# Performance work log

Hardware: AMD Instinct MI355X
Metric: run time of the kernel (lower is better)

## Reference

```python
import jax, jax.numpy as jnp
import numpy as np

B, S, I, H, O = 512, 1024, 1, 2048, 128


def _uniform(k, shape, bound):
    return jax.random.uniform(k, shape, jnp.float32, -bound, bound)


def setup_inputs() -> dict:
    key = jax.random.key(0)
    ks = jax.random.split(key, 12)
    gate_bound = 1.0 / np.sqrt(I + H)  # torch nn.Linear default init range
    out_bound = 1.0 / np.sqrt(H)
    return {
        "x": jax.random.normal(ks[0], (B, S, I), jnp.float32),
        "Wg": _uniform(ks[1], (H, I + H), gate_bound),
        "bg": _uniform(ks[2], (H,), gate_bound),
        "Wi": _uniform(ks[3], (H, I + H), gate_bound),
        "bi": _uniform(ks[4], (H,), gate_bound),
        "Wf": _uniform(ks[5], (H, I + H), gate_bound),
        "bf": _uniform(ks[6], (H,), gate_bound),
        "Wo": _uniform(ks[7], (H, I + H), gate_bound),
        "bo": _uniform(ks[8], (H,), gate_bound),
        "Wy": _uniform(ks[9], (O, H), out_bound),
        "by": _uniform(ks[10], (O,), out_bound),
    }


def reference(x, Wg, bg, Wi, bi, Wf, bf, Wo, bo, Wy, by):
    # Batched, scan-over-time LSTM: same math as the original nested Python
    # loops (zero initial h/c, 4 separate gate Linears on concat([x_t, h]),
    # c = g*i + c*f, h = tanh(c)*o, output Linear on the last h).
    b_, h_dim = x.shape[0], Wg.shape[0]
    # Stack the 4 gate weights -> single fused matmul per step. [4H, I+H]
    W = jnp.concatenate([Wg, Wi, Wf, Wo], axis=0)
    b = jnp.concatenate([bg, bi, bf, bo], axis=0)
    h0 = jnp.zeros((b_, h_dim), x.dtype)
    c0 = jnp.zeros((b_, h_dim), x.dtype)

    def step(carry, xt):
        h, c = carry
        xh = jnp.concatenate([xt, h], axis=-1)  # [B, I+H]
        z = xh @ W.T + b                         # [B, 4H]
        g, i, f, o = jnp.split(z, 4, axis=-1)
        g = jnp.tanh(g)
        i = jax.nn.sigmoid(i)
        f = jax.nn.sigmoid(f)
        o = jax.nn.sigmoid(o)
        c = g * i + c * f
        h = jnp.tanh(c) * o
        return (h, c), None

    xs = jnp.swapaxes(x, 0, 1)  # [S, B, I] time-major for scan
    (h_last, _), _ = jax.lax.scan(step, (h0, c0), xs)
    return h_last @ Wy.T + by  # [B, O]
```

## Files before the change

kernel.cpp:

```cpp
#include <hip/hip_runtime.h>

typedef _Float16 f16;
typedef _Float16 f16x8 __attribute__((ext_vector_type(8)));
typedef float f32x4 __attribute__((ext_vector_type(4)));

static constexpr int kS = 1024;

static constexpr size_t OFF_WP = 0;
static constexpr size_t OFF_WX = 33554432;
static constexpr size_t OFF_BB = OFF_WX + 32768;
static constexpr size_t OFF_XT = OFF_BB + 32768;
static constexpr size_t OFF_HA = OFF_XT + 2097152;
static constexpr size_t OFF_HB = OFF_HA + 2097152;
static constexpr size_t OFF_CB = OFF_HB + 2097152;

__device__ __forceinline__ void gload16(const void* g, void* l) {
  __builtin_amdgcn_global_load_lds(
      (const __attribute__((address_space(1))) unsigned int*)g,
      (__attribute__((address_space(3))) unsigned int*)l, 16, 0, 0);
}

__device__ __forceinline__ float sigf(float x) { return 1.f / (1.f + __expf(-x)); }
__device__ __forceinline__ float tanh_fast(float x) {
  float e = __expf(2.f * x);
  return 1.f - 2.f / (e + 1.f);
}

__global__ void pack_weights(const float* __restrict__ Wg, const float* __restrict__ Wi,
                             const float* __restrict__ Wf, const float* __restrict__ Wo,
                             const float* __restrict__ bg, const float* __restrict__ bi,
                             const float* __restrict__ bf, const float* __restrict__ bo,
                             f16* __restrict__ Wp, float* __restrict__ wx, float* __restrict__ bb)
{
  const int R = blockIdx.x;
  const int p = R >> 8, r = R & 255;
  const int u = (p << 6) + (r >> 2), gsel = r & 3;
  const float* Wsrc = (gsel == 0) ? Wg : (gsel == 1) ? Wi : (gsel == 2) ? Wf : Wo;
  const float* bsrc = (gsel == 0) ? bg : (gsel == 1) ? bi : (gsel == 2) ? bf : bo;
  const float* src = Wsrc + (size_t)u * 2049;
  const int k = threadIdx.x * 8;
#pragma unroll
  for (int j = 0; j < 8; ++j)
    Wp[(size_t)R * 2048 + k + j] = (f16)src[1 + k + j];
  if (threadIdx.x == 0) { wx[R] = src[0]; bb[R] = bsrc[u]; }
}

__global__ void transpose_x(const float* __restrict__ x, float* __restrict__ xT) {
  const int idx = blockIdx.x * 256 + threadIdx.x;
  const int b = idx >> 10, t = idx & 1023;
  xT[t * 512 + b] = x[idx];
}

__global__ void zero_h(f16* hA) {
  const int idx = blockIdx.x * 256 + threadIdx.x;
  ((uint4*)hA)[idx] = make_uint4(0u, 0u, 0u, 0u);
}

__global__ __launch_bounds__(256, 1) void lstm_step(
    const f16* __restrict__ Wp, const float* __restrict__ wx,
    const float* __restrict__ bb, const float* __restrict__ xT,
    const f16* __restrict__ hin, f16* __restrict__ hout,
    float* __restrict__ cbuf, int t)
{
  extern __shared__ __align__(16) char smem[];
  f16* ldsA = (f16*)smem;
  f16* ldsB = (f16*)(smem + 49152);
  f16* ldsH = (f16*)smem;

  const int blk = blockIdx.x;
  const int p  = (blk & 7) + 8 * (blk >> 5);
  const int bp = (blk >> 3) & 3;
  const int u0 = p * 32, b0 = bp * 128;

  const int tid = threadIdx.x;
  const int w = tid >> 6, l = tid & 63;
  const int wr = w >> 1, wc = w & 1;
  const int l15 = l & 15, hi = l >> 4;
  const int r3 = l >> 3, c7 = l & 7;
  const int ksw = (c7 ^ r3) * 8;

  float wxr[4][4], br[4][4];
#pragma unroll
  for (int ni = 0; ni < 4; ++ni)
#pragma unroll
    for (int r = 0; r < 4; ++r) {
      const int R = p * 128 + wr * 64 + ni * 16 + hi * 4 + r;
      wxr[ni][r] = wx[R];
      br[ni][r] = bb[R];
    }

  float xv[4];
#pragma unroll
  for (int bj = 0; bj < 4; ++bj)
    xv[bj] = xT[t * 512 + b0 + wc * 64 + bj * 16 + l15];

  float* cme = cbuf + ((size_t)blk * 256 + tid) * 16;
  float cst[4][4];
  if (t == 0) {
#pragma unroll
    for (int ni = 0; ni < 4; ++ni)
#pragma unroll
      for (int bj = 0; bj < 4; ++bj) cst[ni][bj] = 0.f;
  } else {
#pragma unroll
    for (int ni = 0; ni < 4; ++ni) {
      const f32x4 cv = __builtin_nontemporal_load((const f32x4*)(cme + ni * 4));
      cst[ni][0] = cv[0]; cst[ni][1] = cv[1]; cst[ni][2] = cv[2]; cst[ni][3] = cv[3];
    }
  }

  auto stage = [&](int ch, int buf) {
    const size_t kof = (size_t)ch * 64 + ksw;
#pragma unroll
    for (int j = 0; j < 4; ++j) {
      const int row = w * 32 + j * 8;
      gload16(Wp + (size_t)(p * 128 + row + r3) * 2048 + kof,
              ldsA + buf * 8192 + row * 64);
    }
#pragma unroll
    for (int j = 0; j < 4; ++j) {
      const int row = w * 32 + j * 8;
      gload16(hin + (size_t)(b0 + row + r3) * 2048 + kof,
              ldsB + buf * 8192 + row * 64);
    }
  };

  f32x4 acc[4][4];
#pragma unroll
  for (int ni = 0; ni < 4; ++ni) {
    f32x4 v;
    v[0] = br[ni][0]; v[1] = br[ni][1]; v[2] = br[ni][2]; v[3] = br[ni][3];
#pragma unroll
    for (int bj = 0; bj < 4; ++bj) acc[ni][bj] = v;
  }

  stage(0, 0);
  stage(1, 1);

  int bufc = 0;
#pragma unroll 1
  for (int ch = 0; ch < 32; ++ch) {
    if (ch < 30) {
      int bufs = bufc - 1; if (bufs < 0) bufs = 2;
      stage(ch + 2, bufs);
      asm volatile("s_waitcnt vmcnt(16)" ::: "memory");
    } else if (ch == 30) {
      asm volatile("s_waitcnt vmcnt(8)" ::: "memory");
    } else {
      asm volatile("s_waitcnt vmcnt(0)" ::: "memory");
    }
    __builtin_amdgcn_sched_barrier(0);
    __builtin_amdgcn_s_barrier();
    __builtin_amdgcn_sched_barrier(0);

    const f16* A  = ldsA + bufc * 8192;
    const f16* Bm = ldsB + bufc * 8192;
#pragma unroll
    for (int ks = 0; ks < 2; ++ks) {
      const int sw = ((ks * 4 + hi) ^ c7) * 8;
      f16x8 af[4], bfr[4];
#pragma unroll
      for (int ni = 0; ni < 4; ++ni)
        af[ni] = *(const f16x8*)(A + (wr * 64 + ni * 16 + l15) * 64 + sw);
#pragma unroll
      for (int bj = 0; bj < 4; ++bj)
        bfr[bj] = *(const f16x8*)(Bm + (wc * 64 + bj * 16 + l15) * 64 + sw);
#pragma unroll
      for (int ni = 0; ni < 4; ++ni)
#pragma unroll
        for (int bj = 0; bj < 4; ++bj)
          acc[ni][bj] = __builtin_amdgcn_mfma_f32_16x16x32_f16(af[ni], bfr[bj], acc[ni][bj], 0, 0, 0);
    }

    __builtin_amdgcn_sched_barrier(0);
    __builtin_amdgcn_s_barrier();
    bufc = (bufc == 2) ? 0 : bufc + 1;
  }

#pragma unroll
  for (int ni = 0; ni < 4; ++ni) {
    f32x4 cnew;
#pragma unroll
    for (int bj = 0; bj < 4; ++bj) {
      const f32x4 a = acc[ni][bj];
      const float z0 = a[0] + xv[bj] * wxr[ni][0];
      const float z1 = a[1] + xv[bj] * wxr[ni][1];
      const float z2 = a[2] + xv[bj] * wxr[ni][2];
      const float z3 = a[3] + xv[bj] * wxr[ni][3];
      const float gg = tanh_fast(z0);
      const float ig = sigf(z1);
      const float fg = sigf(z2);
      const float og = sigf(z3);
      const float cc = gg * ig + cst[ni][bj] * fg;
      cnew[bj] = cc;
      const float hh = tanh_fast(cc) * og;
      ldsH[(wc * 64 + bj * 16 + l15) * 40 + (wr * 16 + ni * 4 + hi)] = (f16)hh;
    }
    __builtin_nontemporal_store(cnew, (f32x4*)(cme + ni * 4));
  }
  __syncthreads();

#pragma unroll
  for (int j = 0; j < 2; ++j) {
    const int q = tid + j * 256;
    const int row = q >> 2, uc = q & 3;
    const f16x8 v = *(const f16x8*)(ldsH + row * 40 + uc * 8);
    __builtin_nontemporal_store(v, (f16x8*)(hout + (size_t)(b0 + row) * 2048 + u0 + uc * 8));
  }
}

__global__ void out_proj(const f16* __restrict__ h, const float* __restrict__ Wy,
                         const float* __restrict__ by, float* __restrict__ y)
{
  const int gi = blockIdx.x * 256 + threadIdx.x;
  const int o = gi & 127, b = gi >> 7;
  const f16* hr = h + (size_t)b * 2048;
  const float* wr = Wy + (size_t)o * 2048;
  float acc = 0.f;
  for (int k = 0; k < 2048; k += 8) {
    const f16x8 hv = *(const f16x8*)(hr + k);
    const float4 wa = *(const float4*)(wr + k);
    const float4 wb = *(const float4*)(wr + k + 4);
    acc += (float)hv[0] * wa.x + (float)hv[1] * wa.y + (float)hv[2] * wa.z + (float)hv[3] * wa.w
         + (float)hv[4] * wb.x + (float)hv[5] * wb.y + (float)hv[6] * wb.z + (float)hv[7] * wb.w;
  }
  y[gi] = acc + by[o];
}

extern "C" void kernel_launch(void* const* d_in, const int* in_sizes, int n_in,
                              void* d_out, int out_size, void* d_ws, size_t ws_size,
                              hipStream_t stream)
{
  const float* x  = (const float*)d_in[0];
  const float* Wg = (const float*)d_in[1];
  const float* bg = (const float*)d_in[2];
  const float* Wi = (const float*)d_in[3];
  const float* bi = (const float*)d_in[4];
  const float* Wf = (const float*)d_in[5];
  const float* bf = (const float*)d_in[6];
  const float* Wo = (const float*)d_in[7];
  const float* bo = (const float*)d_in[8];
  const float* Wy = (const float*)d_in[9];
  const float* by = (const float*)d_in[10];
  float* y = (float*)d_out;

  char* ws = (char*)d_ws;
  f16*   Wp = (f16*)(ws + OFF_WP);
  float* wx = (float*)(ws + OFF_WX);
  float* bb = (float*)(ws + OFF_BB);
  float* xT = (float*)(ws + OFF_XT);
  f16*   hA = (f16*)(ws + OFF_HA);
  f16*   hB = (f16*)(ws + OFF_HB);
  float* cb = (float*)(ws + OFF_CB);

  pack_weights<<<8192, 256, 0, stream>>>(Wg, Wi, Wf, Wo, bg, bi, bf, bo, Wp, wx, bb);
  transpose_x<<<2048, 256, 0, stream>>>(x, xT);
  zero_h<<<512, 256, 0, stream>>>(hA);

  (void)hipFuncSetAttribute((const void*)lstm_step,
                            hipFuncAttributeMaxDynamicSharedMemorySize, 131072);
  for (int t = 0; t < kS; ++t) {
    const f16* hin = (t & 1) ? hB : hA;
    f16*      hout = (t & 1) ? hA : hB;
    lstm_step<<<256, 256, 98304, stream>>>(Wp, wx, bb, xT, hin, hout, cb, t);
  }

  out_proj<<<256, 256, 0, stream>>>(hA, Wy, by, y);
}
```

Baseline: 30.26 ms.

## Split LSTM step into 512 smaller-batch tiles with 4-stage K pipeline

```diff
diff --git a/kernel.cpp b/kernel.cpp
--- a/kernel.cpp
+++ b/kernel.cpp
@@ -56,7 +56,7 @@
   ((uint4*)hA)[idx] = make_uint4(0u, 0u, 0u, 0u);
 }
 
-__global__ __launch_bounds__(256, 1) void lstm_step(
+__global__ __launch_bounds__(256, 2) void lstm_step(
     const f16* __restrict__ Wp, const float* __restrict__ wx,
     const float* __restrict__ bb, const float* __restrict__ xT,
     const f16* __restrict__ hin, f16* __restrict__ hout,
@@ -64,88 +64,86 @@
 {
   extern __shared__ __align__(16) char smem[];
   f16* ldsA = (f16*)smem;
-  f16* ldsB = (f16*)(smem + 49152);
+  f16* ldsB = (f16*)(smem + 32768);
   f16* ldsH = (f16*)smem;
 
   const int blk = blockIdx.x;
-  const int p  = (blk & 7) + 8 * (blk >> 5);
-  const int bp = (blk >> 3) & 3;
-  const int u0 = p * 32, b0 = bp * 128;
+  const int c8 = blk & 7, j8 = (blk >> 3) & 7, g8 = blk >> 6;
+  const int wp = g8 * 8 + c8;
+  const int bp = j8;
+  const int b0 = bp * 64, u0 = wp * 32;
 
   const int tid = threadIdx.x;
   const int w = tid >> 6, l = tid & 63;
   const int wr = w >> 1, wc = w & 1;
   const int l15 = l & 15, hi = l >> 4;
-  const int r3 = l >> 3, c7 = l & 7;
-  const int ksw = (c7 ^ r3) * 8;
+  const int usw = (l & 3) ^ ((l >> 3) & 3);
+  const int rg4 = l >> 2;
 
   float wxr[4][4], br[4][4];
 #pragma unroll
   for (int ni = 0; ni < 4; ++ni)
 #pragma unroll
     for (int r = 0; r < 4; ++r) {
-      const int R = p * 128 + wr * 64 + ni * 16 + hi * 4 + r;
+      const int R = wp * 128 + wr * 64 + ni * 16 + hi * 4 + r;
       wxr[ni][r] = wx[R];
       br[ni][r] = bb[R];
     }
 
-  float xv[4];
-#pragma unroll
-  for (int bj = 0; bj < 4; ++bj)
-    xv[bj] = xT[t * 512 + b0 + wc * 64 + bj * 16 + l15];
-
-  float* cme = cbuf + ((size_t)blk * 256 + tid) * 16;
-  float cst[4][4];
+  float xv[2];
+#pragma unroll
+  for (int bj = 0; bj < 2; ++bj)
+    xv[bj] = xT[t * 512 + b0 + wc * 32 + bj * 16 + l15];
+
+  float* cme = cbuf + ((size_t)blk * 256 + tid) * 8;
+  float cst[4][2];
   if (t == 0) {
 #pragma unroll
-    for (int ni = 0; ni < 4; ++ni)
-#pragma unroll
-      for (int bj = 0; bj < 4; ++bj) cst[ni][bj] = 0.f;
+    for (int ni = 0; ni < 4; ++ni) { cst[ni][0] = 0.f; cst[ni][1] = 0.f; }
   } else {
 #pragma unroll
-    for (int ni = 0; ni < 4; ++ni) {
-      const f32x4 cv = __builtin_nontemporal_load((const f32x4*)(cme + ni * 4));
-      cst[ni][0] = cv[0]; cst[ni][1] = cv[1]; cst[ni][2] = cv[2]; cst[ni][3] = cv[3];
-    }
-  }
-
-  auto stage = [&](int ch, int buf) {
-    const size_t kof = (size_t)ch * 64 + ksw;
-#pragma unroll
-    for (int j = 0; j < 4; ++j) {
-      const int row = w * 32 + j * 8;
-      gload16(Wp + (size_t)(p * 128 + row + r3) * 2048 + kof,
-              ldsA + buf * 8192 + row * 64);
-    }
-#pragma unroll
-    for (int j = 0; j < 4; ++j) {
-      const int row = w * 32 + j * 8;
-      gload16(hin + (size_t)(b0 + row + r3) * 2048 + kof,
-              ldsB + buf * 8192 + row * 64);
-    }
+    for (int q = 0; q < 2; ++q) {
+      const f32x4 cv = __builtin_nontemporal_load((const f32x4*)(cme + q * 4));
+#pragma unroll
+      for (int ni = 0; ni < 2; ++ni) {
+        cst[q * 2 + ni][0] = cv[ni * 2 + 0];
+        cst[q * 2 + ni][1] = cv[ni * 2 + 1];
+      }
+    }
+  }
+
+  auto stage = [&](int ch) {
+    const int slot = ch & 3;
+    const size_t kof = (size_t)ch * 32 + usw * 8;
+#pragma unroll
+    for (int jj = 0; jj < 2; ++jj) {
+      const int row = w * 32 + jj * 16;
+      gload16(Wp + (size_t)(wp * 128 + row + rg4) * 2048 + kof,
+              ldsA + slot * 4096 + row * 32);
+    }
+    gload16(hin + (size_t)(b0 + w * 16 + rg4) * 2048 + kof,
+            ldsB + slot * 2048 + w * 16 * 32);
   };
 
-  f32x4 acc[4][4];
+  f32x4 acc[4][2];
 #pragma unroll
   for (int ni = 0; ni < 4; ++ni) {
     f32x4 v;
     v[0] = br[ni][0]; v[1] = br[ni][1]; v[2] = br[ni][2]; v[3] = br[ni][3];
-#pragma unroll
-    for (int bj = 0; bj < 4; ++bj) acc[ni][bj] = v;
-  }
-
-  stage(0, 0);
-  stage(1, 1);
-
-  int bufc = 0;
+    acc[ni][0] = v; acc[ni][1] = v;
+  }
+
+  stage(0); stage(1); stage(2);
+
 #pragma unroll 1
-  for (int ch = 0; ch < 32; ++ch) {
-    if (ch < 30) {
-      int bufs = bufc - 1; if (bufs < 0) bufs = 2;
-      stage(ch + 2, bufs);
-      asm volatile("s_waitcnt vmcnt(16)" ::: "memory");
-    } else if (ch == 30) {
-      asm volatile("s_waitcnt vmcnt(8)" ::: "memory");
+  for (int ch = 0; ch < 64; ++ch) {
+    if (ch < 61) {
+      stage(ch + 3);
+      asm volatile("s_waitcnt vmcnt(9)" ::: "memory");
+    } else if (ch == 61) {
+      asm volatile("s_waitcnt vmcnt(6)" ::: "memory");
+    } else if (ch == 62) {
+      asm volatile("s_waitcnt vmcnt(3)" ::: "memory");
     } else {
       asm volatile("s_waitcnt vmcnt(0)" ::: "memory");
     }
@@ -153,57 +151,57 @@
     __builtin_amdgcn_s_barrier();
     __builtin_amdgcn_sched_barrier(0);
 
-    const f16* A  = ldsA + bufc * 8192;
-    const f16* Bm = ldsB + bufc * 8192;
-#pragma unroll
-    for (int ks = 0; ks < 2; ++ks) {
-      const int sw = ((ks * 4 + hi) ^ c7) * 8;
-      f16x8 af[4], bfr[4];
-#pragma unroll
-      for (int ni = 0; ni < 4; ++ni)
-        af[ni] = *(const f16x8*)(A + (wr * 64 + ni * 16 + l15) * 64 + sw);
-#pragma unroll
-      for (int bj = 0; bj < 4; ++bj)
-        bfr[bj] = *(const f16x8*)(Bm + (wc * 64 + bj * 16 + l15) * 64 + sw);
-#pragma unroll
-      for (int ni = 0; ni < 4; ++ni)
-#pragma unroll
-        for (int bj = 0; bj < 4; ++bj)
-          acc[ni][bj] = __builtin_amdgcn_mfma_f32_16x16x32_f16(af[ni], bfr[bj], acc[ni][bj], 0, 0, 0);
-    }
-
-    __builtin_amdgcn_sched_barrier(0);
-    __builtin_amdgcn_s_barrier();
-    bufc = (bufc == 2) ? 0 : bufc + 1;
-  }
-
-#pragma unroll
-  for (int ni = 0; ni < 4; ++ni) {
+    const f16* A  = ldsA + (ch & 3) * 4096;
+    const f16* Bm = ldsB + (ch & 3) * 2048;
+    f16x8 af[4], bfr[2];
+#pragma unroll
+    for (int ni = 0; ni < 4; ++ni) {
+      const int r = wr * 64 + ni * 16 + l15;
+      const int up = hi ^ ((r >> 1) & 3);
+      af[ni] = *(const f16x8*)(A + r * 32 + up * 8);
+    }
+#pragma unroll
+    for (int bj = 0; bj < 2; ++bj) {
+      const int r = wc * 32 + bj * 16 + l15;
+      const int up = hi ^ ((r >> 1) & 3);
+      bfr[bj] = *(const f16x8*)(Bm + r * 32 + up * 8);
+    }
+#pragma unroll
+    for (int ni = 0; ni < 4; ++ni)
+#pragma unroll
+      for (int bj = 0; bj < 2; ++bj)
+        acc[ni][bj] = __builtin_amdgcn_mfma_f32_16x16x32_f16(af[ni], bfr[bj], acc[ni][bj], 0, 0, 0);
+  }
+
+#pragma unroll
+  for (int q = 0; q < 2; ++q) {
     f32x4 cnew;
 #pragma unroll
-    for (int bj = 0; bj < 4; ++bj) {
-      const f32x4 a = acc[ni][bj];
-      const float z0 = a[0] + xv[bj] * wxr[ni][0];
-      const float z1 = a[1] + xv[bj] * wxr[ni][1];
-      const float z2 = a[2] + xv[bj] * wxr[ni][2];
-      const float z3 = a[3] + xv[bj] * wxr[ni][3];
-      const float gg = tanh_fast(z0);
-      const float ig = sigf(z1);
-      const float fg = sigf(z2);
-      const float og = sigf(z3);
-      const float cc = gg * ig + cst[ni][bj] * fg;
-      cnew[bj] = cc;
-      const float hh = tanh_fast(cc) * og;
-      ldsH[(wc * 64 + bj * 16 + l15) * 40 + (wr * 16 + ni * 4 + hi)] = (f16)hh;
-    }
-    __builtin_nontemporal_store(cnew, (f32x4*)(cme + ni * 4));
+    for (int ni = 0; ni < 2; ++ni) {
+      const int nn = q * 2 + ni;
+#pragma unroll
+      for (int bj = 0; bj < 2; ++bj) {
+        const f32x4 a = acc[nn][bj];
+        const float z0 = a[0] + xv[bj] * wxr[nn][0];
+        const float z1 = a[1] + xv[bj] * wxr[nn][1];
+        const float z2 = a[2] + xv[bj] * wxr[nn][2];
+        const float z3 = a[3] + xv[bj] * wxr[nn][3];
+        const float gg = tanh_fast(z0);
+        const float ig = sigf(z1);
+        const float fg = sigf(z2);
+        const float og = sigf(z3);
+        const float cc = gg * ig + cst[nn][bj] * fg;
+        cnew[ni * 2 + bj] = cc;
+        const float hh = tanh_fast(cc) * og;
+        ldsH[(wc * 32 + bj * 16 + l15) * 40 + (wr * 16 + nn * 4 + hi)] = (f16)hh;
+      }
+    }
+    __builtin_nontemporal_store(cnew, (f32x4*)(cme + q * 4));
   }
   __syncthreads();
 
-#pragma unroll
-  for (int j = 0; j < 2; ++j) {
-    const int q = tid + j * 256;
-    const int row = q >> 2, uc = q & 3;
+  {
+    const int row = tid >> 2, uc = tid & 3;
     const f16x8 v = *(const f16x8*)(ldsH + row * 40 + uc * 8);
     __builtin_nontemporal_store(v, (f16x8*)(hout + (size_t)(b0 + row) * 2048 + u0 + uc * 8));
   }
@@ -258,11 +256,11 @@
   zero_h<<<512, 256, 0, stream>>>(hA);
 
   (void)hipFuncSetAttribute((const void*)lstm_step,
-                            hipFuncAttributeMaxDynamicSharedMemorySize, 131072);
+                            hipFuncAttributeMaxDynamicSharedMemorySize, 65536);
   for (int t = 0; t < kS; ++t) {
     const f16* hin = (t & 1) ? hB : hA;
     f16*      hout = (t & 1) ? hA : hB;
-    lstm_step<<<256, 256, 98304, stream>>>(Wp, wx, bb, xT, hin, hout, cb, t);
+    lstm_step<<<512, 256, 49152, stream>>>(Wp, wx, bb, xT, hin, hout, cb, t);
   }
 
   out_proj<<<256, 256, 0, stream>>>(hA, Wy, by, y);
```

After: 35.02 ms. 1.16x slower.

## Switch recurrent GEMM to FP8 MFMA with scaled weights and hidden state

Applied to the files above, without the earlier changes.

```diff
diff --git a/kernel.cpp b/kernel.cpp
--- a/kernel.cpp
+++ b/kernel.cpp
@@ -3,16 +3,22 @@
 typedef _Float16 f16;
 typedef _Float16 f16x8 __attribute__((ext_vector_type(8)));
 typedef float f32x4 __attribute__((ext_vector_type(4)));
+typedef unsigned int u32x4 __attribute__((ext_vector_type(4)));
+typedef long i64;
 
 static constexpr int kS = 1024;
+static constexpr float WSCALE = 8192.f;
+static constexpr float HSCALE = 64.f;
+static constexpr float ZDESCALE = 1.f / (8192.f * 64.f);
 
 static constexpr size_t OFF_WP = 0;
-static constexpr size_t OFF_WX = 33554432;
+static constexpr size_t OFF_WX = 16777216;
 static constexpr size_t OFF_BB = OFF_WX + 32768;
 static constexpr size_t OFF_XT = OFF_BB + 32768;
-static constexpr size_t OFF_HA = OFF_XT + 2097152;
-static constexpr size_t OFF_HB = OFF_HA + 2097152;
-static constexpr size_t OFF_CB = OFF_HB + 2097152;
+static constexpr size_t OFF_H8A = OFF_XT + 2097152;
+static constexpr size_t OFF_H8B = OFF_H8A + 2097152/2;
+static constexpr size_t OFF_HF  = OFF_H8B + 2097152/2;
+static constexpr size_t OFF_CB  = OFF_HF + 2097152;
 
 __device__ __forceinline__ void gload16(const void* g, void* l) {
   __builtin_amdgcn_global_load_lds(
@@ -25,12 +31,16 @@
   float e = __expf(2.f * x);
   return 1.f - 2.f / (e + 1.f);
 }
+__device__ __forceinline__ unsigned char to_fp8(float v) {
+  return (unsigned char)(__builtin_amdgcn_cvt_pk_fp8_f32(v, 0.f, 0, false) & 0xFF);
+}
 
 __global__ void pack_weights(const float* __restrict__ Wg, const float* __restrict__ Wi,
                              const float* __restrict__ Wf, const float* __restrict__ Wo,
                              const float* __restrict__ bg, const float* __restrict__ bi,
                              const float* __restrict__ bf, const float* __restrict__ bo,
-                             f16* __restrict__ Wp, float* __restrict__ wx, float* __restrict__ bb)
+                             unsigned char* __restrict__ Wp, float* __restrict__ wx,
+                             float* __restrict__ bb)
 {
   const int R = blockIdx.x;
   const int p = R >> 8, r = R & 255;
@@ -39,9 +49,14 @@
   const float* bsrc = (gsel == 0) ? bg : (gsel == 1) ? bi : (gsel == 2) ? bf : bo;
   const float* src = Wsrc + (size_t)u * 2049;
   const int k = threadIdx.x * 8;
-#pragma unroll
-  for (int j = 0; j < 8; ++j)
-    Wp[(size_t)R * 2048 + k + j] = (f16)src[1 + k + j];
+  float v[8];
+#pragma unroll
+  for (int j = 0; j < 8; ++j) v[j] = src[1 + k + j] * WSCALE;
+  int lo = __builtin_amdgcn_cvt_pk_fp8_f32(v[0], v[1], 0, false);
+  lo = __builtin_amdgcn_cvt_pk_fp8_f32(v[2], v[3], lo, true);
+  int hi2 = __builtin_amdgcn_cvt_pk_fp8_f32(v[4], v[5], 0, false);
+  hi2 = __builtin_amdgcn_cvt_pk_fp8_f32(v[6], v[7], hi2, true);
+  *(uint2*)(Wp + (size_t)R * 2048 + k) = make_uint2((unsigned)lo, (unsigned)hi2);
   if (threadIdx.x == 0) { wx[R] = src[0]; bb[R] = bsrc[u]; }
 }
 
@@ -51,21 +66,21 @@
   xT[t * 512 + b] = x[idx];
 }
 
-__global__ void zero_h(f16* hA) {
+__global__ void zero_h(unsigned char* h8) {
   const int idx = blockIdx.x * 256 + threadIdx.x;
-  ((uint4*)hA)[idx] = make_uint4(0u, 0u, 0u, 0u);
+  ((uint4*)h8)[idx] = make_uint4(0u, 0u, 0u, 0u);
 }
 
 __global__ __launch_bounds__(256, 1) void lstm_step(
-    const f16* __restrict__ Wp, const float* __restrict__ wx,
+    const unsigned char* __restrict__ Wp, const float* __restrict__ wx,
     const float* __restrict__ bb, const float* __restrict__ xT,
-    const f16* __restrict__ hin, f16* __restrict__ hout,
-    float* __restrict__ cbuf, int t)
+    const unsigned char* __restrict__ hin, unsigned char* __restrict__ hout,
+    f16* __restrict__ hF, float* __restrict__ cbuf, int t)
 {
   extern __shared__ __align__(16) char smem[];
-  f16* ldsA = (f16*)smem;
-  f16* ldsB = (f16*)(smem + 49152);
-  f16* ldsH = (f16*)smem;
+  unsigned char* ldsA = (unsigned char*)smem;
+  unsigned char* ldsB = (unsigned char*)(smem + 24576);
+  unsigned char* ldsH = (unsigned char*)smem;
 
   const int blk = blockIdx.x;
   const int p  = (blk & 7) + 8 * (blk >> 5);
@@ -76,8 +91,8 @@
   const int w = tid >> 6, l = tid & 63;
   const int wr = w >> 1, wc = w & 1;
   const int l15 = l & 15, hi = l >> 4;
-  const int r3 = l >> 3, c7 = l & 7;
-  const int ksw = (c7 ^ r3) * 8;
+  const int lrow = l >> 2;
+  const int kblk = ((l & 3) ^ (lrow & 3)) * 16;
 
   float wxr[4][4], br[4][4];
 #pragma unroll
@@ -109,43 +124,40 @@
     }
   }
 
-  auto stage = [&](int ch, int buf) {
-    const size_t kof = (size_t)ch * 64 + ksw;
-#pragma unroll
-    for (int j = 0; j < 4; ++j) {
-      const int row = w * 32 + j * 8;
-      gload16(Wp + (size_t)(p * 128 + row + r3) * 2048 + kof,
-              ldsA + buf * 8192 + row * 64);
-    }
-#pragma unroll
-    for (int j = 0; j < 4; ++j) {
-      const int row = w * 32 + j * 8;
-      gload16(hin + (size_t)(b0 + row + r3) * 2048 + kof,
-              ldsB + buf * 8192 + row * 64);
+  auto stage = [&](int ch, int slot) {
+    const size_t kof = (size_t)ch * 64 + kblk;
+#pragma unroll
+    for (int j = 0; j < 2; ++j) {
+      const int rowbase = w * 32 + j * 16;
+      gload16(Wp + (size_t)(p * 128 + rowbase + lrow) * 2048 + kof,
+              ldsA + slot * 8192 + rowbase * 64);
+    }
+#pragma unroll
+    for (int j = 0; j < 2; ++j) {
+      const int rowbase = w * 32 + j * 16;
+      gload16(hin + (size_t)(b0 + rowbase + lrow) * 2048 + kof,
+              ldsB + slot * 8192 + rowbase * 64);
     }
   };
 
   f32x4 acc[4][4];
 #pragma unroll
-  for (int ni = 0; ni < 4; ++ni) {
-    f32x4 v;
-    v[0] = br[ni][0]; v[1] = br[ni][1]; v[2] = br[ni][2]; v[3] = br[ni][3];
-#pragma unroll
-    for (int bj = 0; bj < 4; ++bj) acc[ni][bj] = v;
-  }
-
-  stage(0, 0);
-  stage(1, 1);
+  for (int ni = 0; ni < 4; ++ni)
+#pragma unroll
+    for (int bj = 0; bj < 4; ++bj)
+      acc[ni][bj] = (f32x4){0.f, 0.f, 0.f, 0.f};
+
+  stage(0, 0); stage(1, 1);
 
   int bufc = 0;
 #pragma unroll 1
   for (int ch = 0; ch < 32; ++ch) {
     if (ch < 30) {
-      int bufs = bufc - 1; if (bufs < 0) bufs = 2;
-      stage(ch + 2, bufs);
-      asm volatile("s_waitcnt vmcnt(16)" ::: "memory");
+      int sslot = bufc - 1; if (sslot < 0) sslot = 2;
+      stage(ch + 2, sslot);
+      asm volatile("s_waitcnt vmcnt(8)" ::: "memory");
     } else if (ch == 30) {
-      asm volatile("s_waitcnt vmcnt(8)" ::: "memory");
+      asm volatile("s_waitcnt vmcnt(4)" ::: "memory");
     } else {
       asm volatile("s_waitcnt vmcnt(0)" ::: "memory");
     }
@@ -153,23 +165,27 @@
     __builtin_amdgcn_s_barrier();
     __builtin_amdgcn_sched_barrier(0);
 
-    const f16* A  = ldsA + bufc * 8192;
-    const f16* Bm = ldsB + bufc * 8192;
+    const unsigned char* A  = ldsA + bufc * 8192;
+    const unsigned char* Bm = ldsB + bufc * 8192;
 #pragma unroll
     for (int ks = 0; ks < 2; ++ks) {
-      const int sw = ((ks * 4 + hi) ^ c7) * 8;
-      f16x8 af[4], bfr[4];
+      const int kk = ks * 4 + hi;
+      i64 af[4], bfr[4];
+#pragma unroll
+      for (int ni = 0; ni < 4; ++ni) {
+        const int r = wr * 64 + ni * 16 + l15;
+        af[ni] = *(const i64*)(A + r * 64 + (((kk >> 1) ^ (r & 3)) << 4) + ((kk & 1) << 3));
+      }
+#pragma unroll
+      for (int bj = 0; bj < 4; ++bj) {
+        const int r = wc * 64 + bj * 16 + l15;
+        bfr[bj] = *(const i64*)(Bm + r * 64 + (((kk >> 1) ^ (r & 3)) << 4) + ((kk & 1) << 3));
+      }
 #pragma unroll
       for (int ni = 0; ni < 4; ++ni)
-        af[ni] = *(const f16x8*)(A + (wr * 64 + ni * 16 + l15) * 64 + sw);
-#pragma unroll
-      for (int bj = 0; bj < 4; ++bj)
-        bfr[bj] = *(const f16x8*)(Bm + (wc * 64 + bj * 16 + l15) * 64 + sw);
-#pragma unroll
-      for (int ni = 0; ni < 4; ++ni)
 #pragma unroll
         for (int bj = 0; bj < 4; ++bj)
-          acc[ni][bj] = __builtin_amdgcn_mfma_f32_16x16x32_f16(af[ni], bfr[bj], acc[ni][bj], 0, 0, 0);
+          acc[ni][bj] = __builtin_amdgcn_mfma_f32_16x16x32_fp8_fp8(af[ni], bfr[bj], acc[ni][bj], 0, 0, 0);
     }
 
     __builtin_amdgcn_sched_barrier(0);
@@ -183,10 +199,10 @@
 #pragma unroll
     for (int bj = 0; bj < 4; ++bj) {
       const f32x4 a = acc[ni][bj];
-      const float z0 = a[0] + xv[bj] * wxr[ni][0];
-      const float z1 = a[1] + xv[bj] * wxr[ni][1];
-      const float z2 = a[2] + xv[bj] * wxr[ni][2];
-      const float z3 = a[3] + xv[bj] * wxr[ni][3];
+      const float z0 = a[0] * ZDESCALE + br[ni][0] + xv[bj] * wxr[ni][0];
+      const float z1 = a[1] * ZDESCALE + br[ni][1] + xv[bj] * wxr[ni][1];
+      const float z2 = a[2] * ZDESCALE + br[ni][2] + xv[bj] * wxr[ni][2];
+      const float z3 = a[3] * ZDESCALE + br[ni][3] + xv[bj] * wxr[ni][3];
       const float gg = tanh_fast(z0);
       const float ig = sigf(z1);
       const float fg = sigf(z2);
@@ -194,18 +210,20 @@
       const float cc = gg * ig + cst[ni][bj] * fg;
       cnew[bj] = cc;
       const float hh = tanh_fast(cc) * og;
-      ldsH[(wc * 64 + bj * 16 + l15) * 40 + (wr * 16 + ni * 4 + hi)] = (f16)hh;
+      const int row = wc * 64 + bj * 16 + l15;
+      const int ucol = wr * 16 + ni * 4 + hi;
+      ldsH[row * 48 + ucol] = to_fp8(hh * HSCALE);
+      if (t == kS - 1)
+        hF[(size_t)(b0 + row) * 2048 + u0 + ucol] = (f16)hh;
     }
     __builtin_nontemporal_store(cnew, (f32x4*)(cme + ni * 4));
   }
   __syncthreads();
 
-#pragma unroll
-  for (int j = 0; j < 2; ++j) {
-    const int q = tid + j * 256;
-    const int row = q >> 2, uc = q & 3;
-    const f16x8 v = *(const f16x8*)(ldsH + row * 40 + uc * 8);
-    __builtin_nontemporal_store(v, (f16x8*)(hout + (size_t)(b0 + row) * 2048 + u0 + uc * 8));
+  {
+    const int row = tid >> 1, half = tid & 1;
+    const u32x4 v = *(const u32x4*)(ldsH + row * 48 + half * 16);
+    __builtin_nontemporal_store(v, (u32x4*)(hout + (size_t)(b0 + row) * 2048 + u0 + half * 16));
   }
 }
 
@@ -245,25 +263,26 @@
   float* y = (float*)d_out;
 
   char* ws = (char*)d_ws;
-  f16*   Wp = (f16*)(ws + OFF_WP);
+  unsigned char* Wp  = (unsigned char*)(ws + OFF_WP);
   float* wx = (float*)(ws + OFF_WX);
   float* bb = (float*)(ws + OFF_BB);
   float* xT = (float*)(ws + OFF_XT);
-  f16*   hA = (f16*)(ws + OFF_HA);
-  f16*   hB = (f16*)(ws + OFF_HB);
+  unsigned char* h8A = (unsigned char*)(ws + OFF_H8A);
+  unsigned char* h8B = (unsigned char*)(ws + OFF_H8B);
+  f16*   hF = (f16*)(ws + OFF_HF);
   float* cb = (float*)(ws + OFF_CB);
 
   pack_weights<<<8192, 256, 0, stream>>>(Wg, Wi, Wf, Wo, bg, bi, bf, bo, Wp, wx, bb);
   transpose_x<<<2048, 256, 0, stream>>>(x, xT);
-  zero_h<<<512, 256, 0, stream>>>(hA);
+  zero_h<<<256, 256, 0, stream>>>(h8A);
 
   (void)hipFuncSetAttribute((const void*)lstm_step,
-                            hipFuncAttributeMaxDynamicSharedMemorySize, 131072);
+                            hipFuncAttributeMaxDynamicSharedMemorySize, 65536);
   for (int t = 0; t < kS; ++t) {
-    const f16* hin = (t & 1) ? hB : hA;
-    f16*      hout = (t & 1) ? hA : hB;
-    lstm_step<<<256, 256, 98304, stream>>>(Wp, wx, bb, xT, hin, hout, cb, t);
-  }
-
-  out_proj<<<256, 256, 0, stream>>>(hA, Wy, by, y);
-}
+    const unsigned char* hin = (t & 1) ? h8B : h8A;
+    unsigned char*      hout = (t & 1) ? h8A : h8B;
+    lstm_step<<<256, 256, 49152, stream>>>(Wp, wx, bb, xT, hin, hout, hF, cb, t);
+  }
+
+  out_proj<<<256, 256, 0, stream>>>(hF, Wy, by, y);
+}
```

Result: slower. 33.87 ms (+11.9%).
